# Kernel optimization log

Hardware: AMD Instinct MI355X
Metric: run time of the kernel (lower is better)

Reference implementation:

```python
import jax, jax.numpy as jnp
import numpy as np

TOKENS = 32768
D_MODEL = 4096
N_EXPERTS = 64
BALANCE_LOSS_WEIGHT = 0.1


def setup_inputs() -> dict:
    key = jax.random.key(0)
    kx, kw1, kw2, kn = jax.random.split(key, 4)
    x = jax.random.normal(kx, (TOKENS, D_MODEL), dtype=jnp.float32)
    # torch nn.Linear weight layout: [out_features, in_features]
    w1 = jax.random.normal(kw1, (N_EXPERTS, D_MODEL), dtype=jnp.float32) / np.sqrt(D_MODEL)
    w2 = jax.random.normal(kw2, (N_EXPERTS, N_EXPERTS), dtype=jnp.float32) / np.sqrt(N_EXPERTS)
    # fixed Gumbel noise sample: g = -log(-log(u)), matching gumbel_rsample
    u = jax.random.uniform(kn, (TOKENS, N_EXPERTS), dtype=jnp.float32, minval=1e-8, maxval=1.0)
    noise = -jnp.log(-jnp.log(u))
    return {"x": x, "w1": w1, "w2": w2, "noise": noise}


def reference(x, w1, w2, noise):
    # MLP gate: Linear(d->E, no bias) -> tanh -> Linear(E->E, no bias)
    h = jnp.tanh(x @ w1.T)                       # [T, E]
    logits = h @ w2.T                             # [T, E]
    scores = jax.nn.softmax(logits, axis=1)       # [T, E]
    logits_w_noise = logits + noise               # gumbel-perturbed logits
    top1_indices = jnp.argmax(logits_w_noise, axis=1)   # [T] int
    top1_scores = jnp.max(logits_w_noise, axis=1)       # [T]
    # balance loss
    importance_mean = scores.mean(axis=0)                        # [E]
    load = jnp.bincount(top1_indices, length=N_EXPERTS)          # [E] int
    load_mean = load.astype(scores.dtype) / x.shape[0]           # [E]
    balance_loss = (N_EXPERTS * jnp.sum(importance_mean * load_mean)
                    * BALANCE_LOSS_WEIGHT)
    return (top1_indices, top1_scores, balance_loss, load_mean, importance_mean)
```

## Files before the change

kernel.cpp:

```cpp
#include <hip/hip_runtime.h>
#include <math.h>

#define TOKENS 32768
#define DM 4096
#define NE 64
#define BALW 0.1f

#define TG 64
#define GBLOCKS (TOKENS / TG)

typedef __attribute__((ext_vector_type(8))) short short8;
typedef __attribute__((ext_vector_type(4))) float f32x4;

typedef unsigned short us;

__device__ inline us bf16r(float f) {
  const unsigned u = __float_as_uint(f);
  return (us)((u + 0x7FFFu + ((u >> 16) & 1u)) >> 16);
}
__device__ inline float bf16f(us s) {
  return __uint_as_float(((unsigned)s) << 16);
}
__device__ inline void split8(const float4 v0, const float4 v1, short8& H,
                              short8& M, short8& L) {
  float v[8] = {v0.x, v0.y, v0.z, v0.w, v1.x, v1.y, v1.z, v1.w};
#pragma unroll
  for (int j = 0; j < 8; ++j) {
    const us hs = bf16r(v[j]);
    const float r1 = v[j] - bf16f(hs);
    const us ms = bf16r(r1);
    const float r2 = r1 - bf16f(ms);
    const us ls = bf16r(r2);
    H[j] = (short)hs; M[j] = (short)ms; L[j] = (short)ls;
  }
}

__device__ inline void split8t(const float4 v0, const float4 v1, short8& H,
                               short8& M, short8& L) {
  unsigned u[8], um[8], ul[8];
  const float v[8] = {v0.x, v0.y, v0.z, v0.w, v1.x, v1.y, v1.z, v1.w};
#pragma unroll
  for (int j = 0; j < 8; ++j) {
    u[j] = __float_as_uint(v[j]);
    const float r1 = v[j] - __uint_as_float(u[j] & 0xFFFF0000u);
    um[j] = __float_as_uint(r1);
    const float r2 = r1 - __uint_as_float(um[j] & 0xFFFF0000u);
    ul[j] = __float_as_uint(r2);
  }
  union Cvt { unsigned u4[4]; short8 s8; } h, m, l;
#pragma unroll
  for (int d = 0; d < 4; ++d) {
    h.u4[d] = __builtin_amdgcn_perm(u[2 * d + 1], u[2 * d], 0x07060302u);
    m.u4[d] = __builtin_amdgcn_perm(um[2 * d + 1], um[2 * d], 0x07060302u);
    l.u4[d] = __builtin_amdgcn_perm(ul[2 * d + 1], ul[2 * d], 0x07060302u);
  }
  H = h.s8; M = m.s8; L = l.s8;
}

#define MFMA(a, b, c) __builtin_amdgcn_mfma_f32_16x16x32_bf16(a, b, c, 0, 0, 0)

__global__ void prep_w1_kernel(const float* __restrict__ w1,
                               us* __restrict__ bws) {
  const int kc = blockIdx.x;
  const int tid = threadIdx.x;
  const int ns = tid >> 6;
  const int l = tid & 63;
  const int r = l & 15, g = l >> 4;
  const int n = 16 * ns + r;
  const int kb = 32 * kc + 8 * g;
  const float* src = &w1[(size_t)n * DM + kb];
  const float4 v0 = *reinterpret_cast<const float4*>(src);
  const float4 v1 = *reinterpret_cast<const float4*>(src + 4);
  short8 H, M, L;
  split8(v0, v1, H, M, L);
  us* dst = bws + ((size_t)(kc * 4 + ns) * 3) * 512 + l * 8;
  *reinterpret_cast<short8*>(dst) = H;
  *reinterpret_cast<short8*>(dst + 512) = M;
  *reinterpret_cast<short8*>(dst + 1024) = L;
}

#define TMM 128

template <int SK>
__global__ __launch_bounds__(256, 2) void gemm_mfma_kernel(
    const float* __restrict__ x, const us* __restrict__ bws,
    float* __restrict__ hp) {
  constexpr int KS = DM / SK;
  constexpr int NIT = KS / 32;
  const int tid = threadIdx.x;
  const int kz = blockIdx.x % SK;
  const int mb = blockIdx.x / SK;
  const int w = tid >> 6;
  const int l = tid & 63;
  const int r = l & 15, g = l >> 4;
  const int row0 = mb * TMM + w * 32;
  const int kb0 = kz * KS;

  f32x4 acc[2][4];
#pragma unroll
  for (int i = 0; i < 2; ++i)
#pragma unroll
    for (int j = 0; j < 4; ++j) acc[i][j] = (f32x4)(0.f);

  const float* xA0 = &x[(size_t)(row0 + r) * DM + kb0 + 8 * g];
  const float* xA1 = xA0 + (size_t)16 * DM;
  const us* bb = bws + (size_t)(kb0 / 32) * 12 * 512 + l * 8;

  float4 a00 = *reinterpret_cast<const float4*>(xA0);
  float4 a01 = *reinterpret_cast<const float4*>(xA0 + 4);
  float4 a10 = *reinterpret_cast<const float4*>(xA1);
  float4 a11 = *reinterpret_cast<const float4*>(xA1 + 4);
  short8 bf[4][3];
#pragma unroll
  for (int ns = 0; ns < 4; ++ns)
#pragma unroll
    for (int p = 0; p < 3; ++p)
      bf[ns][p] = *reinterpret_cast<const short8*>(bb + (ns * 3 + p) * 512);

  for (int it = 0; it < NIT; ++it) {
    const int itn = (it + 1 < NIT) ? it + 1 : it;
    const us* btn = bb + (size_t)itn * 12 * 512;
    const int ko = itn * 32;
    const float4 n00 = *reinterpret_cast<const float4*>(xA0 + ko);
    const float4 n01 = *reinterpret_cast<const float4*>(xA0 + ko + 4);
    const float4 n10 = *reinterpret_cast<const float4*>(xA1 + ko);
    const float4 n11 = *reinterpret_cast<const float4*>(xA1 + ko + 4);

    short8 ah0, am0, al0, ah1, am1, al1;
    split8t(a00, a01, ah0, am0, al0);
    split8t(a10, a11, ah1, am1, al1);

#define PROW2(AH0, AH1, P)                                               \
  do {                                                                   \
    _Pragma("unroll") for (int ns = 0; ns < 4; ++ns) {                   \
      acc[0][ns] = MFMA(AH0, bf[ns][P], acc[0][ns]);                     \
      acc[1][ns] = MFMA(AH1, bf[ns][P], acc[1][ns]);                     \
    }                                                                    \
  } while (0)
#define RELOAD(P)                                                        \
  do {                                                                   \
    _Pragma("unroll") for (int ns = 0; ns < 4; ++ns) bf[ns][P] =         \
        *reinterpret_cast<const short8*>(btn + (ns * 3 + (P)) * 512);    \
  } while (0)

    PROW2(ah0, ah1, 0);
    PROW2(am0, am1, 0);
    PROW2(al0, al1, 0);
    RELOAD(0);
    PROW2(ah0, ah1, 1);
    PROW2(am0, am1, 1);
    RELOAD(1);
    PROW2(ah0, ah1, 2);
    RELOAD(2);
#undef PROW2
#undef RELOAD

    a00 = n00; a01 = n01; a10 = n10; a11 = n11;
  }

  float* dst = hp + (size_t)kz * TOKENS * NE;
#pragma unroll
  for (int ms = 0; ms < 2; ++ms)
#pragma unroll
    for (int ns = 0; ns < 4; ++ns)
#pragma unroll
      for (int q = 0; q < 4; ++q)
        dst[(size_t)(row0 + 16 * ms + 4 * g + q) * NE + 16 * ns + r] =
            acc[ms][ns][q];
}

#define TM 128
#define BK 32
#define LDSA 132
#define LDSB 68

template <int SK>
__global__ __launch_bounds__(256, 4) void gemm_fp32_kernel(
    const float* __restrict__ x, const float* __restrict__ w1,
    float* __restrict__ hp) {
  constexpr int KS = DM / SK;
  __shared__ float As[BK * LDSA];
  __shared__ float Ws[BK * LDSB];
  const int tid = threadIdx.x;
  const int kz = blockIdx.x % SK;
  const int mb = blockIdx.x / SK;
  const int row0 = mb * TM;
  const int kbase = kz * KS;
  const int m0 = (tid >> 3) * 4;
  const int n0 = (tid & 7) * 8;
  const int rS = tid >> 2;
  const int kS = (tid & 3) * 4;

  float acc[4][8];
#pragma unroll
  for (int i = 0; i < 4; ++i)
#pragma unroll
    for (int j = 0; j < 8; ++j) acc[i][j] = 0.f;

  float4 ra[4], rw[2];
  const float* xp = &x[(size_t)(row0 + rS) * DM + kS];
  const float* wp = &w1[(size_t)rS * DM + kS];

#define LOAD_TILE(KC)                                                   \
  do {                                                                  \
    ra[0] = *reinterpret_cast<const float4*>(xp + (KC));                \
    ra[1] = *reinterpret_cast<const float4*>(xp + (KC) + 16);           \
    ra[2] = *reinterpret_cast<const float4*>(xp + (size_t)64 * DM + (KC));\
    ra[3] = *reinterpret_cast<const float4*>(xp + (size_t)64 * DM + (KC) + 16);\
    rw[0] = *reinterpret_cast<const float4*>(wp + (KC));                \
    rw[1] = *reinterpret_cast<const float4*>(wp + (KC) + 16);           \
  } while (0)

#define ST4(arr, stride, krow, col, v)                                  \
  do {                                                                  \
    arr[((krow) + 0) * (stride) + (col)] = (v).x;                       \
    arr[((krow) + 1) * (stride) + (col)] = (v).y;                       \
    arr[((krow) + 2) * (stride) + (col)] = (v).z;                       \
    arr[((krow) + 3) * (stride) + (col)] = (v).w;                       \
  } while (0)

#define STORE_TILE()                                                    \
  do {                                                                  \
    ST4(As, LDSA, kS, rS, ra[0]);                                       \
    ST4(As, LDSA, kS + 16, rS, ra[1]);                                  \
    ST4(As, LDSA, kS, rS + 64, ra[2]);                                  \
    ST4(As, LDSA, kS + 16, rS + 64, ra[3]);                             \
    ST4(Ws, LDSB, kS, rS, rw[0]);                                       \
    ST4(Ws, LDSB, kS + 16, rS, rw[1]);                                  \
  } while (0)

  LOAD_TILE(kbase);

  for (int kc = kbase; kc < kbase + KS; kc += BK) {
    __syncthreads();
    STORE_TILE();
    __syncthreads();
    if (kc + BK < kbase + KS) LOAD_TILE(kc + BK);
#pragma unroll 8
    for (int k = 0; k < BK; ++k) {
      const float4 a0 = *reinterpret_cast<const float4*>(&As[k * LDSA + m0]);
      const float4 b0 = *reinterpret_cast<const float4*>(&Ws[k * LDSB + n0]);
      const float4 b1 =
          *reinterpret_cast<const float4*>(&Ws[k * LDSB + n0 + 4]);
      const float a[4] = {a0.x, a0.y, a0.z, a0.w};
      const float b[8] = {b0.x, b0.y, b0.z, b0.w, b1.x, b1.y, b1.z, b1.w};
#pragma unroll
      for (int i = 0; i < 4; ++i)
#pragma unroll
        for (int j = 0; j < 8; ++j) acc[i][j] = fmaf(a[i], b[j], acc[i][j]);
    }
  }
#undef LOAD_TILE
#undef ST4
#undef STORE_TILE

  float* dst = hp + (size_t)kz * TOKENS * NE;
#pragma unroll
  for (int i = 0; i < 4; ++i) {
    const size_t o = (size_t)(row0 + m0 + i) * NE;
    *reinterpret_cast<float4*>(&dst[o + n0]) =
        make_float4(acc[i][0], acc[i][1], acc[i][2], acc[i][3]);
    *reinterpret_cast<float4*>(&dst[o + n0 + 4]) =
        make_float4(acc[i][4], acc[i][5], acc[i][6], acc[i][7]);
  }
}

template <int SK>
__global__ __launch_bounds__(256) void gate_kernel(
    const float* __restrict__ hp, const float* __restrict__ w2,
    const float* __restrict__ noise, float* __restrict__ out_idx,
    float* __restrict__ out_score, float* __restrict__ imp_part,
    float* __restrict__ load_part) {
  __shared__ float hs[TG * 65];
  __shared__ float w2s[NE * 65];
  __shared__ float ls[TG * 66];
  __shared__ float csum[2 * NE];
  __shared__ int hist[NE];
  const int tid = threadIdx.x;
  const int t0 = blockIdx.x * TG;
  if (tid < NE) hist[tid] = 0;

#pragma unroll
  for (int it = 0; it < 4; ++it) {
    const int f = tid + 256 * it;
    const int c = f & 15;
    const int t = f >> 4;
    const size_t g = (size_t)(t0 + t) * NE + c * 4;
    float4 p = *reinterpret_cast<const float4*>(&hp[g]);
#pragma unroll
    for (int s = 1; s < SK; ++s) {
      const float4 q =
          *reinterpret_cast<const float4*>(&hp[(size_t)s * TOKENS * NE + g]);
      p.x += q.x; p.y += q.y; p.z += q.z; p.w += q.w;
    }
    float* d = &hs[t * 65 + c * 4];
    d[0] = tanhf(p.x);
    d[1] = tanhf(p.y);
    d[2] = tanhf(p.z);
    d[3] = tanhf(p.w);
  }
#pragma unroll
  for (int it = 0; it < 4; ++it) {
    const int f = tid + 256 * it;
    const int c = f & 15;
    const int rr = f >> 4;
    const float4 v =
        *reinterpret_cast<const float4*>(&w2[(size_t)rr * NE + c * 4]);
    float* d = &w2s[rr * 65 + c * 4];
    d[0] = v.x; d[1] = v.y; d[2] = v.z; d[3] = v.w;
  }
  __syncthreads();

  {
    const int m0 = (tid >> 4) * 4;
    const int n0 = (tid & 15) * 4;
    float acc[4][4];
#pragma unroll
    for (int i = 0; i < 4; ++i)
#pragma unroll
      for (int j = 0; j < 4; ++j) acc[i][j] = 0.f;
#pragma unroll 8
    for (int k = 0; k < NE; ++k) {
      float a[4], b[4];
#pragma unroll
      for (int i = 0; i < 4; ++i) a[i] = hs[(m0 + i) * 65 + k];
#pragma unroll
      for (int j = 0; j < 4; ++j) b[j] = w2s[(n0 + j) * 65 + k];
#pragma unroll
      for (int i = 0; i < 4; ++i)
#pragma unroll
        for (int j = 0; j < 4; ++j) acc[i][j] = fmaf(a[i], b[j], acc[i][j]);
    }
#pragma unroll
    for (int i = 0; i < 4; ++i)
#pragma unroll
      for (int j = 0; j < 4; ++j) ls[(m0 + i) * 66 + n0 + j] = acc[i][j];
  }
  __syncthreads();

  if (tid < TG) {
    const int t = tid;
    float mx = -INFINITY, best = -INFINITY;
    int bi = 0;
    for (int e = 0; e < NE; ++e) {
      const float lv = ls[t * 66 + e];
      mx = fmaxf(mx, lv);
      const float gg = lv + noise[(size_t)(t0 + t) * NE + e];
      if (gg > best) { best = gg; bi = e; }
    }
    float s = 0.f;
    for (int e = 0; e < NE; ++e) {
      const float ex = expf(ls[t * 66 + e] - mx);
      s += ex;
      ls[t * 66 + e] = ex;
    }
    const float inv = 1.f / s;
    for (int e = 0; e < NE; ++e) ls[t * 66 + e] *= inv;
    out_idx[t0 + t] = (float)bi;
    out_score[t0 + t] = best;
    atomicAdd(&hist[bi], 1);
  }
  __syncthreads();

  if (tid < 128) {
    const int e = tid & 63;
    const int half = tid >> 6;
    float s = 0.f;
    for (int rr = half * 32; rr < half * 32 + 32; ++rr) s += ls[rr * 66 + e];
    csum[half * NE + e] = s;
  }
  __syncthreads();
  if (tid < NE) {
    imp_part[(size_t)blockIdx.x * NE + tid] = csum[tid] + csum[NE + tid];
    load_part[(size_t)blockIdx.x * NE + tid] = (float)hist[tid];
  }
}

__global__ void finalize_kernel(const float* __restrict__ imp_part,
                                const float* __restrict__ load_part,
                                float* __restrict__ out) {
  __shared__ float si[16][NE];
  __shared__ float sl[16][NE];
  const int tid = threadIdx.x;
  const int e = tid & 63;
  const int seg = tid >> 6;
  float imp = 0.f, ld = 0.f;
  for (int b = seg; b < GBLOCKS; b += 16) {
    imp += imp_part[(size_t)b * NE + e];
    ld += load_part[(size_t)b * NE + e];
  }
  si[seg][e] = imp;
  sl[seg][e] = ld;
  __syncthreads();
  if (tid < NE) {
    float ti = 0.f, tl = 0.f;
#pragma unroll
    for (int s = 0; s < 16; ++s) { ti += si[s][tid]; tl += sl[s][tid]; }
    const float imp_mean = ti / (float)TOKENS;
    const float load_mean = tl / (float)TOKENS;
    out[2 * TOKENS + 1 + tid] = load_mean;
    out[2 * TOKENS + 1 + NE + tid] = imp_mean;
    float prod = imp_mean * load_mean;
#pragma unroll
    for (int off = 32; off > 0; off >>= 1) prod += __shfl_down(prod, off);
    if (tid == 0) out[2 * TOKENS] = (float)NE * prod * BALW;
  }
}

extern "C" void kernel_launch(void* const* d_in, const int* in_sizes, int n_in,
                              void* d_out, int out_size, void* d_ws,
                              size_t ws_size, hipStream_t stream) {
  const float* x = (const float*)d_in[0];
  const float* w1 = (const float*)d_in[1];
  const float* w2 = (const float*)d_in[2];
  const float* noise = (const float*)d_in[3];
  float* out = (float*)d_out;

  const size_t bws_shorts = (size_t)128 * 4 * 3 * 512;
  const size_t part_elems = (size_t)2 * GBLOCKS * NE;
  const size_t need_mfma = bws_shorts * sizeof(us) +
                           ((size_t)2 * TOKENS * NE + part_elems) *
                               sizeof(float);
  const size_t need_fp32 =
      ((size_t)2 * TOKENS * NE + part_elems) * sizeof(float);

  if (ws_size == 0 || ws_size >= need_mfma) {
    us* bws = (us*)d_ws;
    float* hp = (float*)(bws + bws_shorts);
    float* imp_part = hp + (size_t)2 * TOKENS * NE;
    float* load_part = imp_part + (size_t)GBLOCKS * NE;
    hipLaunchKernelGGL(prep_w1_kernel, dim3(128), dim3(256), 0, stream, w1,
                       bws);
    hipLaunchKernelGGL((gemm_mfma_kernel<2>), dim3((TOKENS / TMM) * 2),
                       dim3(256), 0, stream, x, bws, hp);
    hipLaunchKernelGGL((gate_kernel<2>), dim3(GBLOCKS), dim3(256), 0, stream,
                       hp, w2, noise, out, out + TOKENS, imp_part, load_part);
    hipLaunchKernelGGL(finalize_kernel, dim3(1), dim3(1024), 0, stream,
                       imp_part, load_part, out);
  } else if (ws_size >= need_fp32) {
    float* hp = (float*)d_ws;
    float* imp_part = hp + (size_t)2 * TOKENS * NE;
    float* load_part = imp_part + (size_t)GBLOCKS * NE;
    hipLaunchKernelGGL((gemm_fp32_kernel<2>), dim3((TOKENS / TM) * 2),
                       dim3(256), 0, stream, x, w1, hp);
    hipLaunchKernelGGL((gate_kernel<2>), dim3(GBLOCKS), dim3(256), 0, stream,
                       hp, w2, noise, out, out + TOKENS, imp_part, load_part);
    hipLaunchKernelGGL(finalize_kernel, dim3(1), dim3(1024), 0, stream,
                       imp_part, load_part, out);
  }
}
```

Before: 200.5 us.

## Prefetch x two iterations ahead with nontemporal loads and MFMA priority

The GEMM kernel now fetches x tiles two k-iterations ahead instead of one, using a rotating register set so global load latency has more time to be hidden. The x loads become nontemporal hints because x is streamed only once. It also raises wave priority around the MFMA groups with s_setprio so compute waves are scheduled ahead of loads. The deeper prefetch adds VGPR pressure under launch_bounds(256,2), which could cause spills or lower occupancy.

Result: slower. 214.0 us (+6.7%).

```diff
diff --git a/kernel.cpp b/kernel.cpp
--- a/kernel.cpp
+++ b/kernel.cpp
@@ -35,10 +35,10 @@
   }
 }
 
-__device__ inline void split8t(const float4 v0, const float4 v1, short8& H,
+__device__ inline void split8t(const f32x4 v0, const f32x4 v1, short8& H,
                                short8& M, short8& L) {
   unsigned u[8], um[8], ul[8];
-  const float v[8] = {v0.x, v0.y, v0.z, v0.w, v1.x, v1.y, v1.z, v1.w};
+  const float v[8] = {v0[0], v0[1], v0[2], v0[3], v1[0], v1[1], v1[2], v1[3]};
 #pragma unroll
   for (int j = 0; j < 8; ++j) {
     u[j] = __float_as_uint(v[j]);
@@ -81,6 +81,8 @@
 
 #define TMM 128
 
+#define NTLOAD(p) __builtin_nontemporal_load(reinterpret_cast<const f32x4*>(p))
+
 template <int SK>
 __global__ __launch_bounds__(256, 2) void gemm_mfma_kernel(
     const float* __restrict__ x, const us* __restrict__ bws,
@@ -106,10 +108,10 @@
   const float* xA1 = xA0 + (size_t)16 * DM;
   const us* bb = bws + (size_t)(kb0 / 32) * 12 * 512 + l * 8;
 
-  float4 a00 = *reinterpret_cast<const float4*>(xA0);
-  float4 a01 = *reinterpret_cast<const float4*>(xA0 + 4);
-  float4 a10 = *reinterpret_cast<const float4*>(xA1);
-  float4 a11 = *reinterpret_cast<const float4*>(xA1 + 4);
+  f32x4 a00 = NTLOAD(xA0), a01 = NTLOAD(xA0 + 4);
+  f32x4 a10 = NTLOAD(xA1), a11 = NTLOAD(xA1 + 4);
+  f32x4 p00 = NTLOAD(xA0 + 32), p01 = NTLOAD(xA0 + 36);
+  f32x4 p10 = NTLOAD(xA1 + 32), p11 = NTLOAD(xA1 + 36);
   short8 bf[4][3];
 #pragma unroll
   for (int ns = 0; ns < 4; ++ns)
@@ -119,12 +121,11 @@
 
   for (int it = 0; it < NIT; ++it) {
     const int itn = (it + 1 < NIT) ? it + 1 : it;
+    const int it2 = (it + 2 < NIT) ? it + 2 : NIT - 1;
     const us* btn = bb + (size_t)itn * 12 * 512;
-    const int ko = itn * 32;
-    const float4 n00 = *reinterpret_cast<const float4*>(xA0 + ko);
-    const float4 n01 = *reinterpret_cast<const float4*>(xA0 + ko + 4);
-    const float4 n10 = *reinterpret_cast<const float4*>(xA1 + ko);
-    const float4 n11 = *reinterpret_cast<const float4*>(xA1 + ko + 4);
+    const int ko2 = it2 * 32;
+    const f32x4 q00 = NTLOAD(xA0 + ko2), q01 = NTLOAD(xA0 + ko2 + 4);
+    const f32x4 q10 = NTLOAD(xA1 + ko2), q11 = NTLOAD(xA1 + ko2 + 4);
 
     short8 ah0, am0, al0, ah1, am1, al1;
     split8t(a00, a01, ah0, am0, al0);
@@ -143,19 +144,26 @@
         *reinterpret_cast<const short8*>(btn + (ns * 3 + (P)) * 512);    \
   } while (0)
 
+    __builtin_amdgcn_s_setprio(1);
     PROW2(ah0, ah1, 0);
     PROW2(am0, am1, 0);
     PROW2(al0, al1, 0);
+    __builtin_amdgcn_s_setprio(0);
     RELOAD(0);
+    __builtin_amdgcn_s_setprio(1);
     PROW2(ah0, ah1, 1);
     PROW2(am0, am1, 1);
+    __builtin_amdgcn_s_setprio(0);
     RELOAD(1);
+    __builtin_amdgcn_s_setprio(1);
     PROW2(ah0, ah1, 2);
+    __builtin_amdgcn_s_setprio(0);
     RELOAD(2);
 #undef PROW2
 #undef RELOAD
 
-    a00 = n00; a01 = n01; a10 = n10; a11 = n11;
+    a00 = p00; a01 = p01; a10 = p10; a11 = p11;
+    p00 = q00; p01 = q01; p10 = q10; p11 = q11;
   }
 
   float* dst = hp + (size_t)kz * TOKENS * NE;
```
